# Kernel optimization log

Measured on AMD Instinct MI355X. Metric: run time of the kernel, lower is better.

Reference implementation:

```python
import jax, jax.numpy as jnp
import numpy as np
import math

N_NEURONS = 2048
TAU_MEM = 10.0
TAU_SYN = 5.0
V_TH = 1.0
V_RESET = 0.0
ALPHA_MEM = math.exp(-1.0 / TAU_MEM)
ALPHA_SYN = math.exp(-1.0 / TAU_SYN)


def setup_inputs() -> dict:
    key = jax.random.key(0)
    B, T, N = 8, 1024, N_NEURONS
    x = jax.random.normal(key, (B, T, N), dtype=jnp.float32)
    membrane = jnp.zeros((B, N), dtype=jnp.float32)
    trace = jnp.zeros((B, N), dtype=jnp.float32)
    return {"x": x, "membrane": membrane, "trace": trace}


def reference(x, membrane, trace):
    """StatefulLIF.forward_sequence: LIF recurrence over T via lax.scan.

    x: [B, T, N]; membrane, trace: [B, N].
    Returns (spikes [B, T, N], final_membrane [B, N], final_trace [B, N]).
    """
    a_m = jnp.asarray(ALPHA_MEM, x.dtype)
    a_s = jnp.asarray(ALPHA_SYN, x.dtype)
    reset_amt = jnp.asarray(V_TH - V_RESET, x.dtype)

    def step(carry, x_t):
        m, tr = carry
        m = a_m * m + (1 - a_m) * x_t
        s = (m > V_TH).astype(x_t.dtype)  # Heaviside spike
        m = m - reset_amt * s
        tr = a_s * tr + s
        return (m, tr), s

    # scan over time: move T to leading axis
    (m_f, tr_f), spikes_t = jax.lax.scan(step, (membrane, trace), jnp.swapaxes(x, 0, 1))
    spikes = jnp.swapaxes(spikes_t, 0, 1)  # [B, T, N]
    return spikes, m_f, tr_f
```

## Files before the change

kernel.cpp:

```cpp
#include <hip/hip_runtime.h>


#define LIF_B 8
#define LIF_T 1024
#define LIF_N 2048

#define A_MEM 0.90483741803595952f
#define A_SYN 0.81873075307798185f

__global__ __launch_bounds__(64) void lif_seq_kernel(
    const float* __restrict__ x,
    const float* __restrict__ m0,
    const float* __restrict__ tr0,
    float* __restrict__ out) {
  const int chain = blockIdx.x * 64 + threadIdx.x;
  const int b = chain >> 11;
  const int n = chain & (LIF_N - 1);

  const size_t plane = (size_t)LIF_T * LIF_N;
  const float* __restrict__ xp = x + (size_t)b * plane + n;
  float* __restrict__ sp = out + (size_t)b * plane + n;

  float m  = m0[chain];
  float tr = tr0[chain];

  constexpr float am   = A_MEM;
  constexpr float as   = A_SYN;
  constexpr float onem = 1.0f - A_MEM;

  constexpr int U = 64;
  float xa[U], xb[U];

  #pragma unroll
  for (int j = 0; j < U; ++j) xa[j] = xp[(size_t)j * LIF_N];
  #pragma unroll
  for (int j = 0; j < U; ++j) xb[j] = xp[(size_t)(U + j) * LIF_N];

  #define LIF_STEP(xv, tt)                                             \
    do {                                                               \
      m = fmaf(am, m, onem * (xv));                                    \
      float s_ = (m > 1.0f) ? 1.0f : 0.0f;               \
      m -= s_;                                      \
      tr = fmaf(as, tr, s_);                                           \
      __builtin_nontemporal_store(s_, &sp[(size_t)(tt) * LIF_N]);      \
    } while (0)

  #pragma unroll 1
  for (int t = 0; t < LIF_T; t += 2 * U) {
    #pragma unroll
    for (int j = 0; j < U; ++j) LIF_STEP(xa[j], t + j);
    if (t + 2 * U < LIF_T) {
      #pragma unroll
      for (int j = 0; j < U; ++j) xa[j] = xp[(size_t)(t + 2 * U + j) * LIF_N];
    }
    #pragma unroll
    for (int j = 0; j < U; ++j) LIF_STEP(xb[j], t + U + j);
    if (t + 3 * U < LIF_T) {
      #pragma unroll
      for (int j = 0; j < U; ++j) xb[j] = xp[(size_t)(t + 3 * U + j) * LIF_N];
    }
  }
  #undef LIF_STEP

  float* mf  = out + (size_t)LIF_B * plane;
  float* trf = mf + (size_t)LIF_B * LIF_N;
  mf[chain]  = m;
  trf[chain] = tr;
}

extern "C" void kernel_launch(void* const* d_in, const int* in_sizes, int n_in,
                              void* d_out, int out_size, void* d_ws, size_t ws_size,
                              hipStream_t stream) {
  const float* x   = (const float*)d_in[0];
  const float* m0  = (const float*)d_in[1];
  const float* tr0 = (const float*)d_in[2];
  float* out = (float*)d_out;

  const int chains = LIF_B * LIF_N;
  const int block = 64;
  const int grid = chains / block;
  lif_seq_kernel<<<grid, block, 0, stream>>>(x, m0, tr0, out);
}
```

Before: 134.2 us.

## Split LIF kernel into producer/consumer waves with LDS double buffering

Each block gets two wavefronts. The producer wave streams x chunks straight into a double-buffered LDS tile using global_load_lds, and the consumer wave reads each chunk from LDS, runs the recurrence and stores the spikes. The aim is to stop the compute wave stalling on global loads and to free the large register arrays of the old design. In exchange it adds a block barrier per chunk and a full vmcnt drain on the producer, uses 32KB of LDS per block, and halves the number of compute lanes per block.

Measured after the change: 123.7 us. 7.8% less time.

```diff
diff --git a/kernel.cpp b/kernel.cpp
--- a/kernel.cpp
+++ b/kernel.cpp
@@ -8,64 +8,93 @@
 #define A_MEM 0.90483741803595952f
 #define A_SYN 0.81873075307798185f
 
-__global__ __launch_bounds__(64) void lif_seq_kernel(
+#define CHUNK 64
+#define NCHUNK (LIF_T / CHUNK)
+
+#define BARRIER()                                  \
+  do {                                             \
+    __asm__ __volatile__("" ::: "memory");         \
+    __builtin_amdgcn_s_barrier();                  \
+    __asm__ __volatile__("" ::: "memory");         \
+  } while (0)
+
+__global__ __launch_bounds__(128) void lif_pc_kernel(
     const float* __restrict__ x,
     const float* __restrict__ m0,
     const float* __restrict__ tr0,
     float* __restrict__ out) {
-  const int chain = blockIdx.x * 64 + threadIdx.x;
+  __shared__ float xbuf[2][CHUNK][64];
+
+  const int wid = threadIdx.x >> 6;
+  const int l   = threadIdx.x & 63;
+  const int chain = blockIdx.x * 64 + l;
   const int b = chain >> 11;
   const int n = chain & (LIF_N - 1);
-
   const size_t plane = (size_t)LIF_T * LIF_N;
   const float* __restrict__ xp = x + (size_t)b * plane + n;
-  float* __restrict__ sp = out + (size_t)b * plane + n;
 
-  float m  = m0[chain];
-  float tr = tr0[chain];
+  if (wid == 0) {
+    #pragma unroll
+    for (int j = 0; j < CHUNK; ++j) {
+      __builtin_amdgcn_global_load_lds(
+          (const __attribute__((address_space(1))) void*)(xp + (size_t)j * LIF_N),
+          (__attribute__((address_space(3))) void*)(&xbuf[0][j][0]),
+          4, 0, 0);
+    }
+    __asm__ __volatile__("s_waitcnt vmcnt(0)" ::: "memory");
+  }
+
+  float m = 0.f, tr = 0.f;
+  float* sp = nullptr;
+  if (wid == 1) {
+    m  = m0[chain];
+    tr = tr0[chain];
+    sp = out + (size_t)b * plane + n;
+  }
+
+  BARRIER();
 
   constexpr float am   = A_MEM;
   constexpr float as   = A_SYN;
   constexpr float onem = 1.0f - A_MEM;
 
-  constexpr int U = 64;
-  float xa[U], xb[U];
+  #pragma unroll 1
+  for (int c = 0; c < NCHUNK; ++c) {
+    if (wid == 0) {
+      if (c + 1 < NCHUNK) {
+        const float* g = xp + (size_t)(c + 1) * CHUNK * LIF_N;
+        #pragma unroll
+        for (int j = 0; j < CHUNK; ++j) {
+          __builtin_amdgcn_global_load_lds(
+              (const __attribute__((address_space(1))) void*)(g + (size_t)j * LIF_N),
+              (__attribute__((address_space(3))) void*)(&xbuf[(c + 1) & 1][j][0]),
+              4, 0, 0);
+        }
+      }
+      __asm__ __volatile__("s_waitcnt vmcnt(0)" ::: "memory");
+    } else {
+      float xr[CHUNK];
+      #pragma unroll
+      for (int j = 0; j < CHUNK; ++j) xr[j] = xbuf[c & 1][j][l];
+      float* spc = sp + (size_t)c * CHUNK * LIF_N;
+      #pragma unroll
+      for (int j = 0; j < CHUNK; ++j) {
+        m = fmaf(am, m, onem * xr[j]);
+        float s_ = (m > 1.0f) ? 1.0f : 0.0f;
+        m -= s_;
+        tr = fmaf(as, tr, s_);
+        __builtin_nontemporal_store(s_, spc + (size_t)j * LIF_N);
+      }
+    }
+    BARRIER();
+  }
 
-  #pragma unroll
-  for (int j = 0; j < U; ++j) xa[j] = xp[(size_t)j * LIF_N];
-  #pragma unroll
-  for (int j = 0; j < U; ++j) xb[j] = xp[(size_t)(U + j) * LIF_N];
-
-  #define LIF_STEP(xv, tt)                                             \
-    do {                                                               \
-      m = fmaf(am, m, onem * (xv));                                    \
-      float s_ = (m > 1.0f) ? 1.0f : 0.0f;               \
-      m -= s_;                                      \
-      tr = fmaf(as, tr, s_);                                           \
-      __builtin_nontemporal_store(s_, &sp[(size_t)(tt) * LIF_N]);      \
-    } while (0)
-
-  #pragma unroll 1
-  for (int t = 0; t < LIF_T; t += 2 * U) {
-    #pragma unroll
-    for (int j = 0; j < U; ++j) LIF_STEP(xa[j], t + j);
-    if (t + 2 * U < LIF_T) {
-      #pragma unroll
-      for (int j = 0; j < U; ++j) xa[j] = xp[(size_t)(t + 2 * U + j) * LIF_N];
-    }
-    #pragma unroll
-    for (int j = 0; j < U; ++j) LIF_STEP(xb[j], t + U + j);
-    if (t + 3 * U < LIF_T) {
-      #pragma unroll
-      for (int j = 0; j < U; ++j) xb[j] = xp[(size_t)(t + 3 * U + j) * LIF_N];
-    }
+  if (wid == 1) {
+    float* mf  = out + (size_t)LIF_B * plane;
+    float* trf = mf + (size_t)LIF_B * LIF_N;
+    mf[chain]  = m;
+    trf[chain] = tr;
   }
-  #undef LIF_STEP
-
-  float* mf  = out + (size_t)LIF_B * plane;
-  float* trf = mf + (size_t)LIF_B * LIF_N;
-  mf[chain]  = m;
-  trf[chain] = tr;
 }
 
 extern "C" void kernel_launch(void* const* d_in, const int* in_sizes, int n_in,
@@ -76,8 +105,6 @@
   const float* tr0 = (const float*)d_in[2];
   float* out = (float*)d_out;
 
-  const int chains = LIF_B * LIF_N;
-  const int block = 64;
-  const int grid = chains / block;
-  lif_seq_kernel<<<grid, block, 0, stream>>>(x, m0, tr0, out);
+  const int grid = (LIF_B * LIF_N) / 64;
+  lif_pc_kernel<<<grid, 128, 0, stream>>>(x, m0, tr0, out);
 }
```
